# Optimization experiments

Hardware: AMD Instinct MI355X
Metric: run time of the kernel (lower is better)

## Reference

```python
import jax, jax.numpy as jnp
import numpy as np

H = 100  # hidden size


def _lstm_final_hidden(x, W_ih, W_hh, b_ih, b_hh):
    # x: [B, T, 4] -> final hidden state h_T: [B, H]
    B, T, _ = x.shape
    # Precompute input contribution for all time steps: [B, T, 4H]
    xW = jnp.einsum('btf,gf->btg', x, W_ih) + b_ih + b_hh
    xW = jnp.transpose(xW, (1, 0, 2))  # [T, B, 4H] for scan over time

    def step(carry, xt):
        h, c = carry
        gates = xt + h @ W_hh.T  # [B, 4H]
        i, f, g, o = jnp.split(gates, 4, axis=-1)  # torch gate order: i, f, g, o
        c = jax.nn.sigmoid(f) * c + jax.nn.sigmoid(i) * jnp.tanh(g)
        h = jax.nn.sigmoid(o) * jnp.tanh(c)
        return (h, c), None

    h0 = jnp.zeros((B, H), dtype=x.dtype)
    (hT, _), _ = jax.lax.scan(step, (h0, h0), xW)
    return hT


def setup_inputs() -> dict:
    key = jax.random.key(0)
    k1, k2, k3, k4, k5 = jax.random.split(key, 5)
    n_cells, T = 4096, 128
    short_ttf = jax.random.normal(k1, (n_cells, 3, T, 4), dtype=jnp.float32)
    W_ih = jax.random.normal(k2, (4 * H, 4), dtype=jnp.float32) * 0.1
    # torch init: uniform(-0.05, 0.05) for weight_hh
    W_hh = jax.random.uniform(k3, (4 * H, H), dtype=jnp.float32, minval=-0.05, maxval=0.05)
    b_ih = jax.random.normal(k4, (4 * H,), dtype=jnp.float32) * 0.1
    b_hh = jax.random.normal(k5, (4 * H,), dtype=jnp.float32) * 0.1
    return {"short_ttf": short_ttf, "W_ih": W_ih, "W_hh": W_hh, "b_ih": b_ih, "b_hh": b_hh}


def reference(short_ttf, W_ih, W_hh, b_ih, b_hh):
    # short_ttf: [n_cells, 3, T, 4]. Each of the 3 sub-sequences per cell is run
    # through the same LSTM; last-step hidden states are concatenated -> [n_cells, 3H].
    n_cells, three, T, F = short_ttf.shape
    x = short_ttf.reshape(n_cells * three, T, F)  # batch all sequences together
    hT = _lstm_final_hidden(x, W_ih, W_hh, b_ih, b_hh)  # [n_cells*3, H]
    return hT.reshape(n_cells, three * H)  # [n_cells, 300]
```

## Files before the change

kernel.cpp:

```cpp
#include <hip/hip_runtime.h>
#include <cstdint>


#define H_UNITS 100
#define T_STEPS 128
#define S_BLK   16
#define NSEQ    12288
#define NBLK    (NSEQ / S_BLK)
#define NTILE   25
#define KSTR    136

typedef __attribute__((ext_vector_type(8))) _Float16 halfx8;
typedef __attribute__((ext_vector_type(8))) unsigned short ushortx8;
typedef __attribute__((ext_vector_type(4))) float floatx4;

__device__ __forceinline__ unsigned short f32_to_f16u(float x) {
    _Float16 h = (_Float16)x;
    return __builtin_bit_cast(unsigned short, h);
}
__device__ __forceinline__ float f16u_to_f32(unsigned short u) {
    _Float16 h = __builtin_bit_cast(_Float16, u);
    return (float)h;
}

__global__ void lstm_prep_pack(const float* __restrict__ W_ih,
                               const float* __restrict__ W_hh,
                               const float* __restrict__ b_ih,
                               const float* __restrict__ b_hh,
                               ushortx8* __restrict__ Bpack) {
    int t = blockIdx.x * 256 + threadIdx.x;
    if (t >= NTILE * 4 * 64) return;
    int lane = t & 63;
    int kc   = (t >> 6) & 3;
    int tile = t >> 8;
    int m    = lane & 15;
    int n  = (m & 3) * 100 + tile * 4 + (m >> 2);
    int k0 = kc * 32 + ((lane >> 4) & 3) * 8;
    ushortx8 v;
#pragma unroll
    for (int j = 0; j < 8; ++j) {
        int k = k0 + j;
        unsigned short w = 0;
        if (k < 100) {
            w = f32_to_f16u(W_hh[n * 100 + k]);
        } else if (k < 108) {
            w = f32_to_f16u(W_ih[n * 4 + ((k - 100) & 3)]);
        } else if (k < 112) {
            float wf = W_ih[n * 4 + (k - 108)];
            unsigned short hi = f32_to_f16u(wf);
            w = f32_to_f16u(wf - f16u_to_f32(hi));
        } else if (k == 112) {
            float b = b_ih[n] + b_hh[n];
            w = f32_to_f16u(b);
        } else if (k == 113) {
            float b = b_ih[n] + b_hh[n];
            unsigned short hi = f32_to_f16u(b);
            w = f32_to_f16u(b - f16u_to_f32(hi));
        }
        v[j] = w;
    }
    Bpack[t] = v;
}

__global__ void __launch_bounds__(256, 3)
lstm_main(const float* __restrict__ x, const ushortx8* __restrict__ Bpack,
          float* __restrict__ out) {
    __shared__ __align__(16) unsigned short s_A[2][16 * KSTR];
    __shared__ __align__(16) ushortx8       s_Wk0[NTILE * 64];

    const int tid  = threadIdx.x;
    const int lane = tid & 63;
    const int wave = tid >> 6;
    const int seq0 = blockIdx.x * S_BLK;
    const int m    = lane & 15;
    const int quad = lane >> 4;

    halfx8 wfrag[7][3];
#pragma unroll
    for (int it = 0; it < 7; ++it) {
        int tile = wave + it * 4;
        if (tile < NTILE) {
#pragma unroll
            for (int kc = 0; kc < 3; ++kc)
                wfrag[it][kc] = __builtin_bit_cast(halfx8, Bpack[(tile * 4 + kc + 1) * 64 + lane]);
        }
    }
    for (int i = tid; i < NTILE * 64; i += 256)
        s_Wk0[i] = Bpack[(i >> 6) * 256 + (i & 63)];

    const int rs = tid & 15, rc = tid >> 4;
    const float* xb = x + (size_t)(seq0 + rs) * (T_STEPS * 4) + (rc & 3);

    for (int i = tid; i < (2 * 16 * KSTR) / 2; i += 256)
        ((unsigned int*)s_A)[i] = 0u;
    float x0 = 0.0f;
    if (tid < 128) x0 = xb[0];
    __syncthreads();
    if (tid < 128) {
        if (rc < 4) {
            unsigned short hi = f32_to_f16u(x0);
            s_A[0][rs * KSTR + 100 + rc] = hi;
            s_A[0][rs * KSTR + 108 + rc] = hi;
        } else {
            float xv = x0;
            unsigned short hi = f32_to_f16u(xv);
            s_A[0][rs * KSTR + 104 + (rc - 4)] = f32_to_f16u(xv - f16u_to_f32(hi));
        }
    } else if (tid < 160) {
        int d = tid - 128;
        s_A[d >> 4][(d & 15) * KSTR + 112] = 0x3C00;
    } else if (tid < 192) {
        int d = tid - 160;
        s_A[d >> 4][(d & 15) * KSTR + 113] = 0x3C00;
    }

    float c_reg[6];
#pragma unroll
    for (int it = 0; it < 6; ++it) c_reg[it] = 0.0f;
    float c24 = 0.0f;

    const int aOff = m * KSTR + quad * 8;

    for (int t = 0; t < T_STEPS; ++t) {
        const int bR = t & 1;
        float xnext = 0.0f;
        if (tid < 128) {
            int tn = t + 1; if (tn > T_STEPS - 1) tn = T_STEPS - 1;
            xnext = xb[tn * 4];
        }
        __syncthreads();

        const unsigned short* base  = s_A[bR];
        unsigned short*       baseW = s_A[bR ^ 1];
        halfx8 hh[4];
#pragma unroll
        for (int kc = 0; kc < 4; ++kc)
            hh[kc] = *(const halfx8*)(base + aOff + kc * 32);

        const bool last = (t == T_STEPS - 1);

        auto docell = [&](int tile, halfx8 w1, halfx8 w2, halfx8 w3, float& cm) {
            halfx8 w0 = __builtin_bit_cast(halfx8, s_Wk0[tile * 64 + lane]);
            floatx4 acc = {0.0f, 0.0f, 0.0f, 0.0f};
            acc = __builtin_amdgcn_mfma_f32_16x16x32_f16(w0, hh[0], acc, 0, 0, 0);
            acc = __builtin_amdgcn_mfma_f32_16x16x32_f16(w1, hh[1], acc, 0, 0, 0);
            acc = __builtin_amdgcn_mfma_f32_16x16x32_f16(w2, hh[2], acc, 0, 0, 0);
            acc = __builtin_amdgcn_mfma_f32_16x16x32_f16(w3, hh[3], acc, 0, 0, 0);
            float ei = __expf(acc[0]);
            float ef = __expf(acc[1]);
            float eg = __expf(2.0f * acc[2]);
            float eo = __expf(acc[3]);
            float a  = 1.0f + ei, b = 1.0f + ef;
            float d  = eg + 1.0f, e2 = eg - 1.0f;
            float q  = a * d;
            float r  = __builtin_amdgcn_rcpf(q * b);
            float nm = fmaf(ef * q, cm, (ei * b) * e2);
            float c  = nm * r;
            cm = c;
            float cc = fminf(c, 40.0f);
            float ec = __expf(2.0f * cc);
            float r2 = __builtin_amdgcn_rcpf((1.0f + eo) * (ec + 1.0f));
            float h  = (eo * (ec - 1.0f)) * r2;
            int j = tile * 4 + quad;
            if (!last) {
                baseW[m * KSTR + j] = f32_to_f16u(h);
            } else {
                out[(size_t)(seq0 + m) * H_UNITS + j] = h;
            }
        };

#pragma unroll
        for (int it = 0; it < 6; ++it)
            docell(wave + it * 4, wfrag[it][0], wfrag[it][1], wfrag[it][2], c_reg[it]);
        if (wave == 0)
            docell(24, wfrag[6][0], wfrag[6][1], wfrag[6][2], c24);

        if (tid < 128 && !last) {
            if (rc < 4) {
                unsigned short hi = f32_to_f16u(xnext);
                baseW[rs * KSTR + 100 + rc] = hi;
                baseW[rs * KSTR + 108 + rc] = hi;
            } else {
                unsigned short hi = f32_to_f16u(xnext);
                baseW[rs * KSTR + 104 + (rc - 4)] = f32_to_f16u(xnext - f16u_to_f32(hi));
            }
        }
        __syncthreads();
    }
}

extern "C" void kernel_launch(void* const* d_in, const int* in_sizes, int n_in,
                              void* d_out, int out_size, void* d_ws, size_t ws_size,
                              hipStream_t stream) {
    const float* x    = (const float*)d_in[0];
    const float* W_ih = (const float*)d_in[1];
    const float* W_hh = (const float*)d_in[2];
    const float* b_ih = (const float*)d_in[3];
    const float* b_hh = (const float*)d_in[4];
    ushortx8* Bpack = (ushortx8*)d_ws;

    lstm_prep_pack<<<25, 256, 0, stream>>>(W_ih, W_hh, b_ih, b_hh, Bpack);
    lstm_main<<<NBLK, 256, 0, stream>>>(x, Bpack, (float*)d_out);
}
```

Baseline: 324.4 us.

## Use five waves per block for balanced tiles and fold log2e into weights

Raises the block from 4 to 5 waves, so the 25 gate tiles split evenly at 5 per wave. Before, wave 0 handled a 7th tile alone and the other waves sat idle for it. The gate weights and biases are also prescaled by log2(e), and by 2·log2(e) for the g gate, so activations can use exp2 directly without multiplies. The cell state is now carried in the scaled domain with a matching clamp. This adds register and occupancy pressure from 320-thread blocks and slightly changes fp16 rounding of the scaled weights.

```diff
diff --git a/kernel.cpp b/kernel.cpp
--- a/kernel.cpp
+++ b/kernel.cpp
@@ -9,6 +9,8 @@
 #define NBLK    (NSEQ / S_BLK)
 #define NTILE   25
 #define KSTR    136
+#define NTHR    320
+#define LOG2E   1.4426950408889634f
 
 typedef __attribute__((ext_vector_type(8))) _Float16 halfx8;
 typedef __attribute__((ext_vector_type(8))) unsigned short ushortx8;
@@ -35,6 +37,7 @@
     int tile = t >> 8;
     int m    = lane & 15;
     int n  = (m & 3) * 100 + tile * 4 + (m >> 2);
+    float sc = (n >= 200 && n < 300) ? (2.0f * LOG2E) : LOG2E;
     int k0 = kc * 32 + ((lane >> 4) & 3) * 8;
     ushortx8 v;
 #pragma unroll
@@ -42,18 +45,18 @@
         int k = k0 + j;
         unsigned short w = 0;
         if (k < 100) {
-            w = f32_to_f16u(W_hh[n * 100 + k]);
+            w = f32_to_f16u(W_hh[n * 100 + k] * sc);
         } else if (k < 108) {
-            w = f32_to_f16u(W_ih[n * 4 + ((k - 100) & 3)]);
+            w = f32_to_f16u(W_ih[n * 4 + ((k - 100) & 3)] * sc);
         } else if (k < 112) {
-            float wf = W_ih[n * 4 + (k - 108)];
+            float wf = W_ih[n * 4 + (k - 108)] * sc;
             unsigned short hi = f32_to_f16u(wf);
             w = f32_to_f16u(wf - f16u_to_f32(hi));
         } else if (k == 112) {
-            float b = b_ih[n] + b_hh[n];
+            float b = (b_ih[n] + b_hh[n]) * sc;
             w = f32_to_f16u(b);
         } else if (k == 113) {
-            float b = b_ih[n] + b_hh[n];
+            float b = (b_ih[n] + b_hh[n]) * sc;
             unsigned short hi = f32_to_f16u(b);
             w = f32_to_f16u(b - f16u_to_f32(hi));
         }
@@ -62,11 +65,11 @@
     Bpack[t] = v;
 }
 
-__global__ void __launch_bounds__(256, 3)
+__global__ void __launch_bounds__(NTHR, 3)
 lstm_main(const float* __restrict__ x, const ushortx8* __restrict__ Bpack,
           float* __restrict__ out) {
     __shared__ __align__(16) unsigned short s_A[2][16 * KSTR];
-    __shared__ __align__(16) ushortx8       s_Wk0[NTILE * 64];
+    __shared__ __align__(16) ushortx8       s_W[NTILE * 64];
 
     const int tid  = threadIdx.x;
     const int lane = tid & 63;
@@ -75,23 +78,21 @@
     const int m    = lane & 15;
     const int quad = lane >> 4;
 
-    halfx8 wfrag[7][3];
-#pragma unroll
-    for (int it = 0; it < 7; ++it) {
-        int tile = wave + it * 4;
-        if (tile < NTILE) {
-#pragma unroll
-            for (int kc = 0; kc < 3; ++kc)
-                wfrag[it][kc] = __builtin_bit_cast(halfx8, Bpack[(tile * 4 + kc + 1) * 64 + lane]);
-        }
-    }
-    for (int i = tid; i < NTILE * 64; i += 256)
-        s_Wk0[i] = Bpack[(i >> 6) * 256 + (i & 63)];
+    halfx8 wfrag[5][3];
+#pragma unroll
+    for (int it = 0; it < 5; ++it) {
+        int tile = wave + it * 5;
+#pragma unroll
+        for (int kc = 0; kc < 3; ++kc)
+            wfrag[it][kc] = __builtin_bit_cast(halfx8, Bpack[(tile * 4 + kc + 1) * 64 + lane]);
+    }
+    for (int i = tid; i < NTILE * 64; i += NTHR)
+        s_W[i] = Bpack[(i >> 6) * 256 + (i & 63)];
 
     const int rs = tid & 15, rc = tid >> 4;
     const float* xb = x + (size_t)(seq0 + rs) * (T_STEPS * 4) + (rc & 3);
 
-    for (int i = tid; i < (2 * 16 * KSTR) / 2; i += 256)
+    for (int i = tid; i < (2 * 16 * KSTR) / 2; i += NTHR)
         ((unsigned int*)s_A)[i] = 0u;
     float x0 = 0.0f;
     if (tid < 128) x0 = xb[0];
@@ -114,10 +115,9 @@
         s_A[d >> 4][(d & 15) * KSTR + 113] = 0x3C00;
     }
 
-    float c_reg[6];
-#pragma unroll
-    for (int it = 0; it < 6; ++it) c_reg[it] = 0.0f;
-    float c24 = 0.0f;
+    float c_reg[5];
+#pragma unroll
+    for (int it = 0; it < 5; ++it) c_reg[it] = 0.0f;
 
     const int aOff = m * KSTR + quad * 8;
 
@@ -139,26 +139,28 @@
 
         const bool last = (t == T_STEPS - 1);
 
-        auto docell = [&](int tile, halfx8 w1, halfx8 w2, halfx8 w3, float& cm) {
-            halfx8 w0 = __builtin_bit_cast(halfx8, s_Wk0[tile * 64 + lane]);
+#pragma unroll
+        for (int it = 0; it < 5; ++it) {
+            int tile = wave + it * 5;
+            halfx8 w0 = __builtin_bit_cast(halfx8, s_W[tile * 64 + lane]);
             floatx4 acc = {0.0f, 0.0f, 0.0f, 0.0f};
-            acc = __builtin_amdgcn_mfma_f32_16x16x32_f16(w0, hh[0], acc, 0, 0, 0);
-            acc = __builtin_amdgcn_mfma_f32_16x16x32_f16(w1, hh[1], acc, 0, 0, 0);
-            acc = __builtin_amdgcn_mfma_f32_16x16x32_f16(w2, hh[2], acc, 0, 0, 0);
-            acc = __builtin_amdgcn_mfma_f32_16x16x32_f16(w3, hh[3], acc, 0, 0, 0);
-            float ei = __expf(acc[0]);
-            float ef = __expf(acc[1]);
-            float eg = __expf(2.0f * acc[2]);
-            float eo = __expf(acc[3]);
+            acc = __builtin_amdgcn_mfma_f32_16x16x32_f16(w0,           hh[0], acc, 0, 0, 0);
+            acc = __builtin_amdgcn_mfma_f32_16x16x32_f16(wfrag[it][0], hh[1], acc, 0, 0, 0);
+            acc = __builtin_amdgcn_mfma_f32_16x16x32_f16(wfrag[it][1], hh[2], acc, 0, 0, 0);
+            acc = __builtin_amdgcn_mfma_f32_16x16x32_f16(wfrag[it][2], hh[3], acc, 0, 0, 0);
+            float ei = exp2f(acc[0]);
+            float ef = exp2f(acc[1]);
+            float eg = exp2f(acc[2]);
+            float eo = exp2f(acc[3]);
             float a  = 1.0f + ei, b = 1.0f + ef;
             float d  = eg + 1.0f, e2 = eg - 1.0f;
             float q  = a * d;
             float r  = __builtin_amdgcn_rcpf(q * b);
-            float nm = fmaf(ef * q, cm, (ei * b) * e2);
-            float c  = nm * r;
-            cm = c;
-            float cc = fminf(c, 40.0f);
-            float ec = __expf(2.0f * cc);
+            float nm = fmaf(ef * q, c_reg[it], (ei * b * (2.0f * LOG2E)) * e2);
+            float c2 = nm * r;
+            c_reg[it] = c2;
+            float cc = fminf(c2, 115.0f);
+            float ec = exp2f(cc);
             float r2 = __builtin_amdgcn_rcpf((1.0f + eo) * (ec + 1.0f));
             float h  = (eo * (ec - 1.0f)) * r2;
             int j = tile * 4 + quad;
@@ -167,13 +169,7 @@
             } else {
                 out[(size_t)(seq0 + m) * H_UNITS + j] = h;
             }
-        };
-
-#pragma unroll
-        for (int it = 0; it < 6; ++it)
-            docell(wave + it * 4, wfrag[it][0], wfrag[it][1], wfrag[it][2], c_reg[it]);
-        if (wave == 0)
-            docell(24, wfrag[6][0], wfrag[6][1], wfrag[6][2], c24);
+        }
 
         if (tid < 128 && !last) {
             if (rc < 4) {
@@ -200,5 +196,5 @@
     ushortx8* Bpack = (ushortx8*)d_ws;
 
     lstm_prep_pack<<<25, 256, 0, stream>>>(W_ih, W_hh, b_ih, b_hh, Bpack);
-    lstm_main<<<NBLK, 256, 0, stream>>>(x, Bpack, (float*)d_out);
-}
+    lstm_main<<<NBLK, NTHR, 0, stream>>>(x, Bpack, (float*)d_out);
+}
```

New measurement: 470.6 us. +45.1%, slower.
